# Kernel tuning notes

Measured on AMD Instinct MI355X. Metric: run time of the kernel, lower is better.

Reference implementation:

```python
import jax, jax.numpy as jnp
import numpy as np

K = 3          # pooling factor (init k)
H_OUT = 8      # number of bilinear heads
H_DIM = 512    # hidden dim after pooling
BN_EPS = 1e-5
NEG_INF = -jnp.inf


def setup_inputs() -> dict:
    key = jax.random.key(0)
    ks = jax.random.split(key, 8)
    b, vn, qn, vd, qd = 16, 256, 256, 512, 768
    hk = H_DIM * K
    return {
        "v": jax.random.normal(ks[0], (b, vn, vd), jnp.float32),
        "q": jax.random.normal(ks[1], (b, qn, qd), jnp.float32),
        "Wv": jax.random.normal(ks[2], (hk, vd), jnp.float32) * 0.05,
        "bv": jax.random.normal(ks[3], (hk,), jnp.float32) * 0.05,
        "Wq": jax.random.normal(ks[4], (hk, qd), jnp.float32) * 0.05,
        "bq": jax.random.normal(ks[5], (hk,), jnp.float32) * 0.05,
        "h_mat": jax.random.normal(ks[6], (1, H_OUT, 1, hk), jnp.float32),
        "h_bias": jax.random.normal(ks[7], (1, H_OUT, 1, 1), jnp.float32),
        "bn_gamma": jnp.ones((H_DIM,), jnp.float32),
        "bn_beta": jnp.zeros((H_DIM,), jnp.float32),
    }


def _forward(v, q, Wv, bv, Wq, bq, h_mat, h_bias, bn_gamma, bn_beta):
    # FCNet (eval mode: dropout is identity; weight_norm folded into W)
    v_ = jax.nn.relu(jnp.einsum("bvd,kd->bvk", v, Wv) + bv)   # [b, vn, h_dim*k]
    q_ = jax.nn.relu(jnp.einsum("bqd,kd->bqk", q, Wq) + bq)   # [b, qn, h_dim*k]

    # Bilinear attention maps: [b, h_out, vn, qn]
    att = jnp.einsum("xhyk,bvk,bqk->bhvq", h_mat, v_, q_) + h_bias

    # v_mask / q_mask (all-zero token rows masked to -inf)
    v_zero = jnp.sum(jnp.abs(v), axis=2) == 0                  # [b, vn]
    q_zero = jnp.sum(jnp.abs(q), axis=2) == 0                  # [b, qn]
    att = jnp.where(v_zero[:, None, :, None], NEG_INF, att)
    att = jnp.where(q_zero[:, None, None, :], NEG_INF, att)

    # Fused per-head attention pooling, summed over heads (original Python loop)
    fused = jnp.einsum("bhvq,bqk->bhvk", att, q_)
    logits_k = jnp.einsum("bvk,bhvk->bk", v_, fused)           # [b, h_dim*k]

    # AvgPool1d(k, stride=k) * k  == sum over groups of k
    b = logits_k.shape[0]
    logits = logits_k.reshape(b, H_DIM, K).sum(axis=2)         # [b, h_dim]

    # BatchNorm1d (training-mode batch statistics, biased variance)
    mu = logits.mean(axis=0)
    var = logits.var(axis=0)
    logits = (logits - mu) * jax.lax.rsqrt(var + BN_EPS) * bn_gamma + bn_beta
    return logits, att


def reference(v, q, Wv, bv, Wq, bq, h_mat, h_bias, bn_gamma, bn_beta):
    return _forward(v, q, Wv, bv, Wq, bq, h_mat, h_bias, bn_gamma, bn_beta)
```

## Files before the change

kernel.cpp:

```cpp
#include <hip/hip_runtime.h>
#include <math.h>

#define BB    16
#define VN    256
#define QN    256
#define VD    512
#define QD    768
#define HK    1536
#define HDIM  512

typedef _Float16 half8 __attribute__((ext_vector_type(8)));
typedef _Float16 half4 __attribute__((ext_vector_type(4)));
typedef float f32x4 __attribute__((ext_vector_type(4)));

__device__ __forceinline__ void lds_barrier() {
    asm volatile("s_waitcnt lgkmcnt(0)" ::: "memory");
    __builtin_amdgcn_s_barrier();
}

__global__ __launch_bounds__(256) void conv_all(
    const float* __restrict__ v, const float* __restrict__ q,
    _Float16* __restrict__ v16in, _Float16* __restrict__ q16in,
    float* __restrict__ vz, float* __restrict__ qz,
    const float* __restrict__ Wv, _Float16* __restrict__ Wv16,
    const float* __restrict__ Wq, _Float16* __restrict__ Wq16,
    const float* __restrict__ hm, _Float16* __restrict__ hs16) {
    int g = blockIdx.x;
    int t = threadIdx.x;
    if (g < 2048) {
        int which = g >> 10;
        int gb = g & 1023;
        const float* src = which ? q : v;
        _Float16* dst = which ? q16in : v16in;
        float* outz = which ? qz : vz;
        int D = which ? QD : VD;
        int w = t >> 6, ln = t & 63;
        int row = gb * 4 + w;
        const float* p = src + (size_t)row * D;
        _Float16* d = dst + (size_t)row * D;
        float s = 0.f;
        for (int c = ln * 4; c < D; c += 256) {
            float4 x = *(const float4*)(p + c);
            s += fabsf(x.x) + fabsf(x.y) + fabsf(x.z) + fabsf(x.w);
            half4 hh = {(_Float16)x.x, (_Float16)x.y, (_Float16)x.z, (_Float16)x.w};
            *(half4*)(d + c) = hh;
        }
        for (int off = 32; off > 0; off >>= 1) s += __shfl_down(s, off);
        if (ln == 0) outz[row] = (s == 0.f) ? 1.f : 0.f;
        return;
    }
    if (g < 3968) {
        int isq = (g >= 2816);
        int gb = isq ? (g - 2816) : (g - 2048);
        const float* src = isq ? Wq : Wv;
        _Float16* dst = isq ? Wq16 : Wv16;
        int n4 = isq ? (HK * QD / 4) : (HK * VD / 4);
        int i = gb * 256 + t;
        if (i < n4) {
            float4 x = ((const float4*)src)[i];
            half4 h = {(_Float16)x.x, (_Float16)x.y, (_Float16)x.z, (_Float16)x.w};
            ((half4*)dst)[i] = h;
        }
        return;
    }
    {
        int k = (g - 3968) * 256 + t;
        if (k >= HK) return;
        float s = 0.f;
#pragma unroll
        for (int h = 0; h < 8; ++h) {
            float x = hm[h * HK + k];
            s += x;
            hs16[h * HK + k] = (_Float16)x;
        }
        hs16[8 * HK + k] = (_Float16)s;
    }
}

__global__ __launch_bounds__(256, 2) void proj128(
    const _Float16* __restrict__ v16in, const _Float16* __restrict__ Wv16,
    const float* __restrict__ bv, _Float16* __restrict__ v16,
    const _Float16* __restrict__ q16in, const _Float16* __restrict__ Wq16,
    const float* __restrict__ bq, _Float16* __restrict__ q16) {
    __shared__ _Float16 As[128 * 64];
    __shared__ _Float16 Bs[128 * 64];
    int lin = blockIdx.x;
    int gg = (lin & 7) * 96 + (lin >> 3);
    int z = gg / 384;
    int r = gg - z * 384;
    int m0 = (r / 12) * 128, n0 = (r % 12) * 128;
    const _Float16* Ain = z ? q16in : v16in;
    const _Float16* W16 = z ? Wq16 : Wv16;
    const float* bias = z ? bq : bv;
    _Float16* C16 = z ? q16 : v16;
    int K = z ? QD : VD;
    int t = threadIdx.x;
    int w = t >> 6, ln = t & 63, quad = ln >> 4, r16 = ln & 15;
    int wi = w & 1, wj = w >> 1;
    int arow = t >> 3, aseg = t & 7;
    int sg = (aseg ^ (arow & 7)) * 8;
    const _Float16* ApG = Ain + (size_t)(m0 + arow) * K + aseg * 8;
    const _Float16* BpG = W16 + (size_t)(n0 + arow) * K + aseg * 8;
    half8 ra[4], rb[4];
#pragma unroll
    for (int c = 0; c < 4; ++c) {
        ra[c] = *(const half8*)(ApG + (size_t)c * 32 * K);
        rb[c] = *(const half8*)(BpG + (size_t)c * 32 * K);
    }
    f32x4 acc[4][4] = {};
    for (int k0 = 0; k0 < K; k0 += 64) {
        lds_barrier();
#pragma unroll
        for (int c = 0; c < 4; ++c) {
            *(half8*)&As[(c * 32 + arow) * 64 + sg] = ra[c];
            *(half8*)&Bs[(c * 32 + arow) * 64 + sg] = rb[c];
        }
        lds_barrier();
        if (k0 + 64 < K) {
#pragma unroll
            for (int c = 0; c < 4; ++c) {
                ra[c] = *(const half8*)(ApG + (size_t)c * 32 * K + k0 + 64);
                rb[c] = *(const half8*)(BpG + (size_t)c * 32 * K + k0 + 64);
            }
        }
#pragma unroll
        for (int kc = 0; kc < 2; ++kc) {
            half8 af[4], bf[4];
#pragma unroll
            for (int fi = 0; fi < 4; ++fi) {
                int rl = wi * 64 + fi * 16 + r16;
                af[fi] = *(const half8*)&As[rl * 64 + ((kc * 4 + quad) ^ (rl & 7)) * 8];
            }
#pragma unroll
            for (int fj = 0; fj < 4; ++fj) {
                int rl = wj * 64 + fj * 16 + r16;
                bf[fj] = *(const half8*)&Bs[rl * 64 + ((kc * 4 + quad) ^ (rl & 7)) * 8];
            }
#pragma unroll
            for (int fi = 0; fi < 4; ++fi)
#pragma unroll
                for (int fj = 0; fj < 4; ++fj)
                    acc[fi][fj] = __builtin_amdgcn_mfma_f32_16x16x32_f16(
                        af[fi], bf[fj], acc[fi][fj], 0, 0, 0);
        }
    }
#pragma unroll
    for (int fi = 0; fi < 4; ++fi) {
#pragma unroll
        for (int r2 = 0; r2 < 4; ++r2) {
            int m = m0 + wi * 64 + fi * 16 + quad * 4 + r2;
#pragma unroll
            for (int fj = 0; fj < 4; ++fj) {
                int n = n0 + wj * 64 + fj * 16 + r16;
                float x = acc[fi][fj][r2] + bias[n];
                C16[(size_t)m * HK + n] = (_Float16)fmaxf(x, 0.f);
            }
        }
    }
}

__global__ __launch_bounds__(256, 2) void att_db(
    const _Float16* __restrict__ v16, const _Float16* __restrict__ q16,
    const _Float16* __restrict__ hs16, const float* __restrict__ hb,
    const float* __restrict__ vz, const float* __restrict__ qz,
    float* __restrict__ att_out, _Float16* __restrict__ A16) {
    __shared__ _Float16 As[2][64 * 64];
    __shared__ _Float16 Bs[2][32 * 64];
    __shared__ _Float16 Hl[8 * HK];
    int lin = blockIdx.x;
    int swz = ((lin & 7) << 6) | (lin >> 3);
    int jb = swz & 7, ib = (swz >> 3) & 3, b = swz >> 5;
    int i0 = ib * 64, j0 = jb * 32;
    int t = threadIdx.x;
    int w = t >> 6, ln = t & 63, quad = ln >> 4, r16 = ln & 15;
    int iw = w & 1, hg = w >> 1, h0 = hg * 4;
    int arow = t >> 3, aseg = t & 7;
    int sg = (aseg ^ (arow & 7)) * 8;
    for (int u = t * 8; u < 8 * HK; u += 256 * 8)
        *(half8*)&Hl[u] = *(const half8*)(hs16 + u);
    const _Float16* ApG = v16 + (size_t)b * VN * HK + (size_t)(i0 + arow) * HK + aseg * 8;
    const _Float16* BpG = q16 + (size_t)b * QN * HK + (size_t)(j0 + arow) * HK + aseg * 8;
    half8 ra[2], rb;
    ra[0] = *(const half8*)(ApG);
    ra[1] = *(const half8*)(ApG + (size_t)32 * HK);
    rb    = *(const half8*)(BpG);
    *(half8*)&As[0][arow * 64 + sg] = ra[0];
    *(half8*)&As[0][(arow + 32) * 64 + sg] = ra[1];
    *(half8*)&Bs[0][arow * 64 + sg] = rb;
    ra[0] = *(const half8*)(ApG + 64);
    ra[1] = *(const half8*)(ApG + (size_t)32 * HK + 64);
    rb    = *(const half8*)(BpG + 64);
    f32x4 acc[4][2][2] = {};
    for (int it = 0; it < 24; ++it) {
        lds_barrier();
        int cur = it & 1;
        const _Float16* Ac = As[cur];
        const _Float16* Bc = Bs[cur];
        if (it + 1 < 24) {
            int nxt = cur ^ 1;
            *(half8*)&As[nxt][arow * 64 + sg] = ra[0];
            *(half8*)&As[nxt][(arow + 32) * 64 + sg] = ra[1];
            *(half8*)&Bs[nxt][arow * 64 + sg] = rb;
        }
        if (it + 2 < 24) {
            int kn = (it + 2) * 64;
            ra[0] = *(const half8*)(ApG + kn);
            ra[1] = *(const half8*)(ApG + (size_t)32 * HK + kn);
            rb    = *(const half8*)(BpG + kn);
        }
        int kb = it * 64;
#pragma unroll
        for (int kc = 0; kc < 2; ++kc) {
            half8 af[2], bf[2];
#pragma unroll
            for (int fi = 0; fi < 2; ++fi) {
                int rl = iw * 32 + fi * 16 + r16;
                af[fi] = *(const half8*)&Ac[rl * 64 + ((kc * 4 + quad) ^ (rl & 7)) * 8];
            }
#pragma unroll
            for (int fj = 0; fj < 2; ++fj) {
                int rl = fj * 16 + r16;
                bf[fj] = *(const half8*)&Bc[rl * 64 + ((kc * 4 + quad) ^ (rl & 7)) * 8];
            }
#pragma unroll
            for (int hh = 0; hh < 4; ++hh) {
                half8 hmv = *(const half8*)&Hl[(h0 + hh) * HK + kb + (kc * 4 + quad) * 8];
#pragma unroll
                for (int fi = 0; fi < 2; ++fi) {
                    half8 am = af[fi] * hmv;
#pragma unroll
                    for (int fj = 0; fj < 2; ++fj)
                        acc[hh][fi][fj] = __builtin_amdgcn_mfma_f32_16x16x32_f16(
                            am, bf[fj], acc[hh][fi][fj], 0, 0, 0);
                }
            }
        }
    }
    float s[2][2][4];
#pragma unroll
    for (int fi = 0; fi < 2; ++fi)
#pragma unroll
        for (int fj = 0; fj < 2; ++fj)
#pragma unroll
            for (int r = 0; r < 4; ++r) {
                float ss = 0.f;
#pragma unroll
                for (int hh = 0; hh < 4; ++hh) ss += acc[hh][fi][fj][r];
                s[fi][fj][r] = ss;
            }
    float hbv[4];
#pragma unroll
    for (int hh = 0; hh < 4; ++hh) hbv[hh] = hb[h0 + hh];
    float hbsum = 0.f;
#pragma unroll
    for (int h = 0; h < 8; ++h) hbsum += hb[h];
    float qm[2];
#pragma unroll
    for (int fj = 0; fj < 2; ++fj) qm[fj] = qz[b * QN + j0 + fj * 16 + r16];
    float* outb = att_out + (size_t)b * 8 * VN * QN;
#pragma unroll
    for (int fi = 0; fi < 2; ++fi) {
#pragma unroll
        for (int r = 0; r < 4; ++r) {
            int i = i0 + iw * 32 + fi * 16 + quad * 4 + r;
            float vm = vz[b * VN + i];
#pragma unroll
            for (int fj = 0; fj < 2; ++fj) {
                int j = j0 + fj * 16 + r16;
                bool msk = (vm != 0.f) || (qm[fj] != 0.f);
#pragma unroll
                for (int hh = 0; hh < 4; ++hh) {
                    float x = acc[hh][fi][fj][r] + hbv[hh];
                    if (msk) x = -INFINITY;
                    outb[(size_t)(h0 + hh) * VN * QN + (size_t)i * QN + j] = x;
                }
            }
        }
    }
    __syncthreads();
    float* Red = (float*)&As[0][0];
    if (hg) {
#pragma unroll
        for (int fi = 0; fi < 2; ++fi)
#pragma unroll
            for (int fj = 0; fj < 2; ++fj)
#pragma unroll
                for (int r = 0; r < 4; ++r)
                    Red[iw * 1024 + (fi * 16 + quad * 4 + r) * 32 + fj * 16 + r16] =
                        s[fi][fj][r];
    }
    __syncthreads();
    if (!hg) {
        _Float16* Ab = A16 + (size_t)b * VN * QN;
#pragma unroll
        for (int fi = 0; fi < 2; ++fi) {
#pragma unroll
            for (int r = 0; r < 4; ++r) {
                int i = i0 + iw * 32 + fi * 16 + quad * 4 + r;
                float vm = vz[b * VN + i];
#pragma unroll
                for (int fj = 0; fj < 2; ++fj) {
                    int j = j0 + fj * 16 + r16;
                    float tot = s[fi][fj][r] +
                                Red[iw * 1024 + (fi * 16 + quad * 4 + r) * 32 + fj * 16 + r16] +
                                hbsum;
                    if (vm != 0.f || qm[fj] != 0.f) tot = -INFINITY;
                    Ab[(size_t)i * QN + j] = (_Float16)tot;
                }
            }
        }
    }
}

__global__ __launch_bounds__(256) void t_lk_ft(
    const _Float16* __restrict__ A16, const _Float16* __restrict__ q16,
    const _Float16* __restrict__ v16, float* __restrict__ lk) {
    __shared__ _Float16 As[256 * 32];
    __shared__ _Float16 Bs[64 * 32];
    __shared__ float red[16][64];
    int b = blockIdx.y;
    int k0 = blockIdx.x * 64;
    int t = threadIdx.x;
    int w = t >> 6, ln = t & 63, quad = ln >> 4, r16 = ln & 15;
    const _Float16* Ab = A16 + (size_t)b * VN * QN;
    const _Float16* Qb = q16 + (size_t)b * QN * HK;
    int ar = t >> 2, aseg = t & 3;
    int tj = t & 31, tk = t >> 5;
    f32x4 acc[4][4] = {};
    for (int j0 = 0; j0 < QN; j0 += 32) {
        half8 a0 = *(const half8*)(Ab + (size_t)(ar +   0) * QN + j0 + aseg * 8);
        half8 a1 = *(const half8*)(Ab + (size_t)(ar +  64) * QN + j0 + aseg * 8);
        half8 a2 = *(const half8*)(Ab + (size_t)(ar + 128) * QN + j0 + aseg * 8);
        half8 a3 = *(const half8*)(Ab + (size_t)(ar + 192) * QN + j0 + aseg * 8);
        half8 q8 = *(const half8*)(Qb + (size_t)(j0 + tj) * HK + k0 + tk * 8);
        __syncthreads();
        *(half8*)&As[(ar +   0) * 32 + aseg * 8] = a0;
        *(half8*)&As[(ar +  64) * 32 + aseg * 8] = a1;
        *(half8*)&As[(ar + 128) * 32 + aseg * 8] = a2;
        *(half8*)&As[(ar + 192) * 32 + aseg * 8] = a3;
#pragma unroll
        for (int e = 0; e < 8; ++e)
            Bs[(tk * 8 + e) * 32 + tj] = q8[e];
        __syncthreads();
        half8 af[4], bf[4];
#pragma unroll
        for (int fi = 0; fi < 4; ++fi)
            af[fi] = *(const half8*)&As[(w * 64 + fi * 16 + r16) * 32 + quad * 8];
#pragma unroll
        for (int fj = 0; fj < 4; ++fj)
            bf[fj] = *(const half8*)&Bs[(fj * 16 + r16) * 32 + quad * 8];
#pragma unroll
        for (int fi = 0; fi < 4; ++fi)
#pragma unroll
            for (int fj = 0; fj < 4; ++fj)
                acc[fi][fj] = __builtin_amdgcn_mfma_f32_16x16x32_f16(
                    af[fi], bf[fj], acc[fi][fj], 0, 0, 0);
    }
    const _Float16* Vb = v16 + (size_t)b * VN * HK;
    float part[4] = {0.f, 0.f, 0.f, 0.f};
#pragma unroll
    for (int fi = 0; fi < 4; ++fi) {
#pragma unroll
        for (int r = 0; r < 4; ++r) {
            int i = w * 64 + fi * 16 + quad * 4 + r;
#pragma unroll
            for (int fj = 0; fj < 4; ++fj) {
                float vv = (float)Vb[(size_t)i * HK + k0 + fj * 16 + r16];
                part[fj] += acc[fi][fj][r] * vv;
            }
        }
    }
#pragma unroll
    for (int fj = 0; fj < 4; ++fj)
        red[w * 4 + quad][fj * 16 + r16] = part[fj];
    __syncthreads();
    if (t < 64) {
        float s = 0.f;
#pragma unroll
        for (int g = 0; g < 16; ++g) s += red[g][t];
        lk[b * HK + k0 + t] = s;
    }
}

__global__ __launch_bounds__(256) void bn_kernel(
    const float* __restrict__ lk, const float* __restrict__ gamma,
    const float* __restrict__ beta, float* __restrict__ out) {
    int d = blockIdx.x * blockDim.x + threadIdx.x;
    if (d >= HDIM) return;
    float l[BB];
    float mu = 0.f;
#pragma unroll
    for (int b = 0; b < BB; ++b) {
        const float* p = lk + b * HK + 3 * d;
        float s = p[0] + p[1] + p[2];
        l[b] = s;
        mu += s;
    }
    mu *= (1.f / BB);
    float var = 0.f;
#pragma unroll
    for (int b = 0; b < BB; ++b) {
        float dd = l[b] - mu;
        var += dd * dd;
    }
    var *= (1.f / BB);
    float inv = rsqrtf(var + 1e-5f);
    float g = gamma[d], be = beta[d];
#pragma unroll
    for (int b = 0; b < BB; ++b)
        out[b * HDIM + d] = (l[b] - mu) * inv * g + be;
}

extern "C" void kernel_launch(void* const* d_in, const int* in_sizes, int n_in,
                              void* d_out, int out_size, void* d_ws, size_t ws_size,
                              hipStream_t stream) {
    const float* v  = (const float*)d_in[0];
    const float* q  = (const float*)d_in[1];
    const float* Wv = (const float*)d_in[2];
    const float* bv = (const float*)d_in[3];
    const float* Wq = (const float*)d_in[4];
    const float* bq = (const float*)d_in[5];
    const float* hm = (const float*)d_in[6];
    const float* hb = (const float*)d_in[7];
    const float* gamma = (const float*)d_in[8];
    const float* beta  = (const float*)d_in[9];

    float* out_logits = (float*)d_out;
    float* out_att    = out_logits + BB * HDIM;

    _Float16* h = (_Float16*)d_ws;
    _Float16* v16   = h;
    _Float16* q16   = v16 + (size_t)BB * VN * HK;
    _Float16* A16   = q16 + (size_t)BB * QN * HK;
    _Float16* v16in = A16 + (size_t)BB * VN * QN;
    _Float16* q16in = v16in + (size_t)BB * VN * VD;
    _Float16* Wv16  = q16in + (size_t)BB * QN * QD;
    _Float16* Wq16  = Wv16 + (size_t)HK * VD;
    _Float16* hs16  = Wq16 + (size_t)HK * QD;
    float* lk = (float*)(hs16 + 9 * HK + 8);
    float* vz = lk + BB * HK;
    float* qz = vz + BB * VN;

    conv_all<<<dim3(3974), 256, 0, stream>>>(
        v, q, v16in, q16in, vz, qz, Wv, Wv16, Wq, Wq16, hm, hs16);

    proj128<<<dim3(768), 256, 0, stream>>>(
        v16in, Wv16, bv, v16, q16in, Wq16, bq, q16);

    att_db<<<dim3(512), 256, 0, stream>>>(
        v16, q16, hs16, hb, vz, qz, out_att, A16);

    t_lk_ft<<<dim3(HK / 64, BB), 256, 0, stream>>>(A16, q16, v16, lk);

    bn_kernel<<<dim3((HDIM + 255) / 256), 256, 0, stream>>>(lk, gamma, beta, out_logits);
}
```

Before: 171.4 us.

## Repartition attention kernel warps over two heads each with 32x64 tiles

Changes the att kernel tiling from 64x32 (i x j) tiles with warps split over row halves and 4-head groups to 32x64 tiles where each of the 4 warps covers the full tile for 2 heads. The aim is to reduce the per-head Hadamard multiplies and per-warp A-fragment work, and to reuse more B fragments per A load. The cross-head sum now goes through a dedicated 3-slot LDS reduction buffer, which adds LDS usage (24KB) and so may affect occupancy. The extra __syncthreads before the reduction is removed.

```diff
diff --git a/kernel.cpp b/kernel.cpp
--- a/kernel.cpp
+++ b/kernel.cpp
@@ -159,38 +159,39 @@
     }
 }
 
-__global__ __launch_bounds__(256, 2) void att_db(
+__global__ __launch_bounds__(256, 2) void att_2h(
     const _Float16* __restrict__ v16, const _Float16* __restrict__ q16,
     const _Float16* __restrict__ hs16, const float* __restrict__ hb,
     const float* __restrict__ vz, const float* __restrict__ qz,
     float* __restrict__ att_out, _Float16* __restrict__ A16) {
-    __shared__ _Float16 As[2][64 * 64];
-    __shared__ _Float16 Bs[2][32 * 64];
+    __shared__ _Float16 As[2][32 * 64];
+    __shared__ _Float16 Bs[2][64 * 64];
     __shared__ _Float16 Hl[8 * HK];
+    __shared__ float Red[3][32 * 64];
     int lin = blockIdx.x;
     int swz = ((lin & 7) << 6) | (lin >> 3);
-    int jb = swz & 7, ib = (swz >> 3) & 3, b = swz >> 5;
-    int i0 = ib * 64, j0 = jb * 32;
+    int jb = swz & 3, ib = (swz >> 2) & 7, b = swz >> 5;
+    int i0 = ib * 32, j0 = jb * 64;
     int t = threadIdx.x;
-    int w = t >> 6, ln = t & 63, quad = ln >> 4, r16 = ln & 15;
-    int iw = w & 1, hg = w >> 1, h0 = hg * 4;
+    int hg = t >> 6, ln = t & 63, quad = ln >> 4, r16 = ln & 15;
+    int h0 = hg * 2;
     int arow = t >> 3, aseg = t & 7;
     int sg = (aseg ^ (arow & 7)) * 8;
     for (int u = t * 8; u < 8 * HK; u += 256 * 8)
         *(half8*)&Hl[u] = *(const half8*)(hs16 + u);
     const _Float16* ApG = v16 + (size_t)b * VN * HK + (size_t)(i0 + arow) * HK + aseg * 8;
     const _Float16* BpG = q16 + (size_t)b * QN * HK + (size_t)(j0 + arow) * HK + aseg * 8;
-    half8 ra[2], rb;
-    ra[0] = *(const half8*)(ApG);
-    ra[1] = *(const half8*)(ApG + (size_t)32 * HK);
-    rb    = *(const half8*)(BpG);
-    *(half8*)&As[0][arow * 64 + sg] = ra[0];
-    *(half8*)&As[0][(arow + 32) * 64 + sg] = ra[1];
-    *(half8*)&Bs[0][arow * 64 + sg] = rb;
-    ra[0] = *(const half8*)(ApG + 64);
-    ra[1] = *(const half8*)(ApG + (size_t)32 * HK + 64);
-    rb    = *(const half8*)(BpG + 64);
-    f32x4 acc[4][2][2] = {};
+    half8 ra, rb[2];
+    ra    = *(const half8*)(ApG);
+    rb[0] = *(const half8*)(BpG);
+    rb[1] = *(const half8*)(BpG + (size_t)32 * HK);
+    *(half8*)&As[0][arow * 64 + sg] = ra;
+    *(half8*)&Bs[0][arow * 64 + sg] = rb[0];
+    *(half8*)&Bs[0][(arow + 32) * 64 + sg] = rb[1];
+    ra    = *(const half8*)(ApG + 64);
+    rb[0] = *(const half8*)(BpG + 64);
+    rb[1] = *(const half8*)(BpG + (size_t)32 * HK + 64);
+    f32x4 acc[2][2][4] = {};
     for (int it = 0; it < 24; ++it) {
         lds_barrier();
         int cur = it & 1;
@@ -198,78 +199,74 @@
         const _Float16* Bc = Bs[cur];
         if (it + 1 < 24) {
             int nxt = cur ^ 1;
-            *(half8*)&As[nxt][arow * 64 + sg] = ra[0];
-            *(half8*)&As[nxt][(arow + 32) * 64 + sg] = ra[1];
-            *(half8*)&Bs[nxt][arow * 64 + sg] = rb;
+            *(half8*)&As[nxt][arow * 64 + sg] = ra;
+            *(half8*)&Bs[nxt][arow * 64 + sg] = rb[0];
+            *(half8*)&Bs[nxt][(arow + 32) * 64 + sg] = rb[1];
         }
         if (it + 2 < 24) {
             int kn = (it + 2) * 64;
-            ra[0] = *(const half8*)(ApG + kn);
-            ra[1] = *(const half8*)(ApG + (size_t)32 * HK + kn);
-            rb    = *(const half8*)(BpG + kn);
+            ra    = *(const half8*)(ApG + kn);
+            rb[0] = *(const half8*)(BpG + kn);
+            rb[1] = *(const half8*)(BpG + (size_t)32 * HK + kn);
         }
         int kb = it * 64;
 #pragma unroll
         for (int kc = 0; kc < 2; ++kc) {
-            half8 af[2], bf[2];
+            half8 af[2], bf[4];
 #pragma unroll
             for (int fi = 0; fi < 2; ++fi) {
-                int rl = iw * 32 + fi * 16 + r16;
+                int rl = fi * 16 + r16;
                 af[fi] = *(const half8*)&Ac[rl * 64 + ((kc * 4 + quad) ^ (rl & 7)) * 8];
             }
 #pragma unroll
-            for (int fj = 0; fj < 2; ++fj) {
+            for (int fj = 0; fj < 4; ++fj) {
                 int rl = fj * 16 + r16;
                 bf[fj] = *(const half8*)&Bc[rl * 64 + ((kc * 4 + quad) ^ (rl & 7)) * 8];
             }
 #pragma unroll
-            for (int hh = 0; hh < 4; ++hh) {
+            for (int hh = 0; hh < 2; ++hh) {
                 half8 hmv = *(const half8*)&Hl[(h0 + hh) * HK + kb + (kc * 4 + quad) * 8];
 #pragma unroll
                 for (int fi = 0; fi < 2; ++fi) {
                     half8 am = af[fi] * hmv;
 #pragma unroll
-                    for (int fj = 0; fj < 2; ++fj)
+                    for (int fj = 0; fj < 4; ++fj)
                         acc[hh][fi][fj] = __builtin_amdgcn_mfma_f32_16x16x32_f16(
                             am, bf[fj], acc[hh][fi][fj], 0, 0, 0);
                 }
             }
         }
     }
-    float s[2][2][4];
+    float s[2][4][4];
 #pragma unroll
     for (int fi = 0; fi < 2; ++fi)
 #pragma unroll
-        for (int fj = 0; fj < 2; ++fj)
-#pragma unroll
-            for (int r = 0; r < 4; ++r) {
-                float ss = 0.f;
-#pragma unroll
-                for (int hh = 0; hh < 4; ++hh) ss += acc[hh][fi][fj][r];
-                s[fi][fj][r] = ss;
-            }
-    float hbv[4];
-#pragma unroll
-    for (int hh = 0; hh < 4; ++hh) hbv[hh] = hb[h0 + hh];
+        for (int fj = 0; fj < 4; ++fj)
+#pragma unroll
+            for (int r = 0; r < 4; ++r)
+                s[fi][fj][r] = acc[0][fi][fj][r] + acc[1][fi][fj][r];
+    float hbv[2];
+#pragma unroll
+    for (int hh = 0; hh < 2; ++hh) hbv[hh] = hb[h0 + hh];
     float hbsum = 0.f;
 #pragma unroll
     for (int h = 0; h < 8; ++h) hbsum += hb[h];
-    float qm[2];
-#pragma unroll
-    for (int fj = 0; fj < 2; ++fj) qm[fj] = qz[b * QN + j0 + fj * 16 + r16];
+    float qm[4];
+#pragma unroll
+    for (int fj = 0; fj < 4; ++fj) qm[fj] = qz[b * QN + j0 + fj * 16 + r16];
     float* outb = att_out + (size_t)b * 8 * VN * QN;
 #pragma unroll
     for (int fi = 0; fi < 2; ++fi) {
 #pragma unroll
         for (int r = 0; r < 4; ++r) {
-            int i = i0 + iw * 32 + fi * 16 + quad * 4 + r;
+            int i = i0 + fi * 16 + quad * 4 + r;
             float vm = vz[b * VN + i];
 #pragma unroll
-            for (int fj = 0; fj < 2; ++fj) {
+            for (int fj = 0; fj < 4; ++fj) {
                 int j = j0 + fj * 16 + r16;
                 bool msk = (vm != 0.f) || (qm[fj] != 0.f);
 #pragma unroll
-                for (int hh = 0; hh < 4; ++hh) {
+                for (int hh = 0; hh < 2; ++hh) {
                     float x = acc[hh][fi][fj][r] + hbv[hh];
                     if (msk) x = -INFINITY;
                     outb[(size_t)(h0 + hh) * VN * QN + (size_t)i * QN + j] = x;
@@ -277,16 +274,14 @@
             }
         }
     }
-    __syncthreads();
-    float* Red = (float*)&As[0][0];
     if (hg) {
 #pragma unroll
         for (int fi = 0; fi < 2; ++fi)
 #pragma unroll
-            for (int fj = 0; fj < 2; ++fj)
+            for (int fj = 0; fj < 4; ++fj)
 #pragma unroll
                 for (int r = 0; r < 4; ++r)
-                    Red[iw * 1024 + (fi * 16 + quad * 4 + r) * 32 + fj * 16 + r16] =
+                    Red[hg - 1][(fi * 16 + quad * 4 + r) * 64 + fj * 16 + r16] =
                         s[fi][fj][r];
     }
     __syncthreads();
@@ -296,14 +291,13 @@
         for (int fi = 0; fi < 2; ++fi) {
 #pragma unroll
             for (int r = 0; r < 4; ++r) {
-                int i = i0 + iw * 32 + fi * 16 + quad * 4 + r;
+                int i = i0 + fi * 16 + quad * 4 + r;
                 float vm = vz[b * VN + i];
 #pragma unroll
-                for (int fj = 0; fj < 2; ++fj) {
+                for (int fj = 0; fj < 4; ++fj) {
                     int j = j0 + fj * 16 + r16;
-                    float tot = s[fi][fj][r] +
-                                Red[iw * 1024 + (fi * 16 + quad * 4 + r) * 32 + fj * 16 + r16] +
-                                hbsum;
+                    int ri = (fi * 16 + quad * 4 + r) * 64 + fj * 16 + r16;
+                    float tot = s[fi][fj][r] + Red[0][ri] + Red[1][ri] + Red[2][ri] + hbsum;
                     if (vm != 0.f || qm[fj] != 0.f) tot = -INFINITY;
                     Ab[(size_t)i * QN + j] = (_Float16)tot;
                 }
@@ -447,7 +441,7 @@
     proj128<<<dim3(768), 256, 0, stream>>>(
         v16in, Wv16, bv, v16, q16in, Wq16, bq, q16);
 
-    att_db<<<dim3(512), 256, 0, stream>>>(
+    att_2h<<<dim3(512), 256, 0, stream>>>(
         v16, q16, hs16, hb, vz, qz, out_att, A16);
 
     t_lk_ft<<<dim3(HK / 64, BB), 256, 0, stream>>>(A16, q16, v16, lk);
```

New measurement: 169.1 us. About the same (-1.4%).
